# Performance work log

Hardware: AMD Instinct MI355X
Metric: run time of the kernel (lower is better)

## Reference

```python
import jax, jax.numpy as jnp
import numpy as np
from jax import lax

EPS = 1e-10

def _safe_norm(x):
    # torch remove_zeros: replace exact-zero norms with 1e-10
    n = jnp.linalg.norm(x, axis=-1, keepdims=True)
    return jnp.where(n != 0, n, jnp.full_like(n, EPS))

def setup_inputs() -> dict:
    key = jax.random.key(0)
    ks = jax.random.split(key, 5)
    S, B, D = 2048, 32, 512  # seq, batch, 2*hidden
    K = 147  # odd(max_entries/14)
    return {
        "encoder_outputs": jax.random.normal(ks[0], (S, B, D), dtype=jnp.float32),
        "state": jax.random.normal(ks[1], (B, D), dtype=jnp.float32),
        "previous_attention": jax.random.uniform(ks[2], (B, S), dtype=jnp.float32),
        "W_att": jax.random.normal(ks[3], (D, D), dtype=jnp.float32) / np.sqrt(D),
        "b_att": jax.random.normal(ks[4], (D,), dtype=jnp.float32) * 0.01,
        "conv_w": jnp.ones((1, 1, K), dtype=jnp.float32),
        "conv_b": jnp.zeros((1,), dtype=jnp.float32),
    }

def reference(encoder_outputs, state, previous_attention, W_att, b_att, conv_w, conv_b):
    S, B, D = encoder_outputs.shape
    # attended state via linear layer, then cosine-similarity weights (vectorized over seq)
    attended = state @ W_att.T + b_att                       # [B, D]
    ns = attended / _safe_norm(attended)                     # [B, D]
    ne = encoder_outputs / _safe_norm(encoder_outputs)       # [S, B, D]
    weights = jnp.einsum('bd,sbd->bs', ns, ne)               # [B, S]
    # conv1d time smoothing of previous attention (same-length, odd kernel)
    k = conv_w.shape[-1]
    pad = k // 2
    y = lax.conv_general_dilated(previous_attention[:, None, :], conv_w,
                                 window_strides=(1,), padding=[(pad, pad)])
    adjusted = jax.nn.relu(y[:, 0, :] + conv_b)              # [B, S]
    prev_probs = adjusted / jnp.sum(adjusted, axis=1, keepdims=True)
    adj = prev_probs * jax.nn.softmax(weights, axis=1)
    norm_w = adj / jnp.sum(adj, axis=1, keepdims=True)       # [B, S]
    applied = jnp.einsum('bs,sbd->bd', norm_w, encoder_outputs)  # [B, D]
    return applied, norm_w
```

## Files before the change

kernel.cpp:

```cpp
#include <hip/hip_runtime.h>
#include <math.h>


__device__ __forceinline__ float wave_sum(float v) {
    for (int off = 32; off; off >>= 1) v += __shfl_xor(v, off);
    return v;
}

__global__ __launch_bounds__(256) void front_kernel(
    const float* __restrict__ state, const float* __restrict__ W,
    const float* __restrict__ bias, const float* __restrict__ prev,
    const float* __restrict__ cw, const float* __restrict__ cb,
    float* __restrict__ attended, float* __restrict__ adj,
    int S, int D, int K) {
    __shared__ __align__(16) float smem[1024];
    int b = blockIdx.y;
    int t = threadIdx.x;

    if (blockIdx.x < 2) {
        if (t < D / 4)
            ((float4*)smem)[t] = ((const float4*)(state + (size_t)b * D))[t];
        __syncthreads();
        int d = blockIdx.x * 256 + t;
        const float4* Wrow = (const float4*)(W + (size_t)d * D);
        const float4* sv = (const float4*)smem;
        float acc = bias[d];
#pragma unroll 8
        for (int k = 0; k < 128; ++k) {
            float4 w4 = Wrow[k];
            float4 s4 = sv[k];
            acc += w4.x * s4.x + w4.y * s4.y + w4.z * s4.z + w4.w * s4.w;
        }
        attended[(size_t)b * D + d] = acc;
    } else {
        int s0 = (blockIdx.x - 2) * 256;
        int pad = K / 2;
        int seglen = 256 + K - 1;
        float* seg = smem;
        float* wk = smem + 512;
        for (int i = t; i < seglen; i += 256) {
            int s = s0 - pad + i;
            seg[i] = (s >= 0 && s < S) ? prev[(size_t)b * S + s] : 0.f;
        }
        for (int j = t; j < K; j += 256) wk[j] = cw[j];
        __syncthreads();
        float y = cb[0];
        for (int j = 0; j < K; ++j) y += seg[t + j] * wk[j];
        adj[(size_t)b * S + s0 + t] = fmaxf(y, 0.f);
    }
}

__global__ __launch_bounds__(256) void main_kernel(
    const float* __restrict__ e, const float* __restrict__ attended,
    const float* __restrict__ adj, float* __restrict__ partial,
    float* __restrict__ zbuf, float* __restrict__ u,
    int S, int B, int D, int CH) {
    __shared__ __align__(16) float reds[4 * 512 + 4];
    int wave = threadIdx.x >> 6;
    int lane = threadIdx.x & 63;
    int c = blockIdx.x * 4 + wave;
    int b = blockIdx.y;

    const float4* att4 = (const float4*)(attended + (size_t)b * D);
    float4 a0 = att4[lane];
    float4 a1 = att4[lane + 64];
    float asq = a0.x * a0.x + a0.y * a0.y + a0.z * a0.z + a0.w * a0.w
              + a1.x * a1.x + a1.y * a1.y + a1.z * a1.z + a1.w * a1.w;
    asq = wave_sum(asq);
    float an = sqrtf(asq);
    if (an == 0.f) an = 1e-10f;
    float ainv = 1.f / an;
    float4 ns0, ns1;
    ns0.x = a0.x * ainv; ns0.y = a0.y * ainv; ns0.z = a0.z * ainv; ns0.w = a0.w * ainv;
    ns1.x = a1.x * ainv; ns1.y = a1.y * ainv; ns1.z = a1.z * ainv; ns1.w = a1.w * ainv;

    int s0 = c * CH;

    float adjv = 0.f;
    if (CH <= 64 && lane < CH) adjv = adj[(size_t)b * S + s0 + lane];

    float4 acc0 = {0.f, 0.f, 0.f, 0.f};
    float4 acc1 = {0.f, 0.f, 0.f, 0.f};
    float z = 0.f;

    const float4* row4 = (const float4*)(e + ((size_t)s0 * B + b) * D);
    size_t rstride = (size_t)B * D / 4;

    float4 x0 = row4[lane];
    float4 x1 = row4[lane + 64];
    for (int i = 0; i < CH; ++i) {
        float4 nx0, nx1;
        if (i + 1 < CH) {
            nx0 = row4[rstride + lane];
            nx1 = row4[rstride + lane + 64];
        }
        float dot = x0.x * ns0.x + x0.y * ns0.y + x0.z * ns0.z + x0.w * ns0.w
                  + x1.x * ns1.x + x1.y * ns1.y + x1.z * ns1.z + x1.w * ns1.w;
        float sq  = x0.x * x0.x + x0.y * x0.y + x0.z * x0.z + x0.w * x0.w
                  + x1.x * x1.x + x1.y * x1.y + x1.z * x1.z + x1.w * x1.w;
        dot = wave_sum(dot);
        sq  = wave_sum(sq);
        float n = sqrtf(sq);
        if (n == 0.f) n = 1e-10f;
        float w = dot / n;
        float av = (CH <= 64) ? __shfl(adjv, i) : adj[(size_t)b * S + s0 + i];
        float coef = av * __expf(w);
        if (lane == 0) u[(size_t)b * S + s0 + i] = coef;
        acc0.x += coef * x0.x; acc0.y += coef * x0.y;
        acc0.z += coef * x0.z; acc0.w += coef * x0.w;
        acc1.x += coef * x1.x; acc1.y += coef * x1.y;
        acc1.z += coef * x1.z; acc1.w += coef * x1.w;
        z += coef;
        x0 = nx0; x1 = nx1;
        row4 += rstride;
    }

    float* wsl = reds + (wave << 9);
    ((float4*)wsl)[lane] = acc0;
    ((float4*)wsl)[lane + 64] = acc1;
    if (lane == 0) reds[2048 + wave] = z;
    __syncthreads();
    int t = threadIdx.x;
    if (t < 128) {
        const float4* r4 = (const float4*)reds;
        float4 v0 = r4[t];
        float4 v1 = r4[t + 128];
        float4 v2 = r4[t + 256];
        float4 v3 = r4[t + 384];
        float4 o;
        o.x = v0.x + v1.x + v2.x + v3.x;
        o.y = v0.y + v1.y + v2.y + v3.y;
        o.z = v0.z + v1.z + v2.z + v3.z;
        o.w = v0.w + v1.w + v2.w + v3.w;
        ((float4*)(partial + ((size_t)blockIdx.x * B + b) * D))[t] = o;
    }
    if (t == 0)
        zbuf[(size_t)blockIdx.x * B + b] =
            reds[2048] + reds[2049] + reds[2050] + reds[2051];
}

__global__ __launch_bounds__(256) void combine_kernel(
    const float* __restrict__ partial, const float* __restrict__ zbuf,
    const float* __restrict__ u, float* __restrict__ applied,
    float* __restrict__ norm_w, int S, int B, int D, int NPART) {
    int q = blockIdx.x;
    int b = blockIdx.y;
    int t = threadIdx.x;
    __shared__ __align__(16) float4 red4[8][32];
    __shared__ float zsh;

    float zt = (t < NPART) ? zbuf[(size_t)t * B + b] : 0.f;
    zt = wave_sum(zt);
    if (t == 0) zsh = 1.f / zt;

    int c2 = t >> 5;
    int di = t & 31;
    int d4 = q * 32 + di;
    const float4* p4 = (const float4*)partial;
    float4 a = {0.f, 0.f, 0.f, 0.f};
#pragma unroll
    for (int k = 0; k < 4; ++k) {
        float4 x = p4[((size_t)(c2 + (k << 3)) * B + b) * (D >> 2) + d4];
        a.x += x.x; a.y += x.y; a.z += x.z; a.w += x.w;
    }
    red4[c2][di] = a;
    __syncthreads();
    float inv = zsh;
    if (t < 32) {
        float4 s = red4[0][t];
#pragma unroll
        for (int j = 1; j < 8; ++j) {
            float4 x = red4[j][t];
            s.x += x.x; s.y += x.y; s.z += x.z; s.w += x.w;
        }
        s.x *= inv; s.y *= inv; s.z *= inv; s.w *= inv;
        ((float4*)(applied + (size_t)b * D))[q * 32 + t] = s;
    }

    const float4* u4 = (const float4*)(u + (size_t)b * S);
    float4* nw4 = (float4*)(norm_w + (size_t)b * S);
    if (t < 128) {
        int idx = q * (S >> 4) + t;
        float4 x = u4[idx];
        x.x *= inv; x.y *= inv; x.z *= inv; x.w *= inv;
        nw4[idx] = x;
    }
}

extern "C" void kernel_launch(void* const* d_in, const int* in_sizes, int n_in,
                              void* d_out, int out_size, void* d_ws, size_t ws_size,
                              hipStream_t stream) {
    const float* enc   = (const float*)d_in[0];
    const float* state = (const float*)d_in[1];
    const float* prev  = (const float*)d_in[2];
    const float* W     = (const float*)d_in[3];
    const float* bias  = (const float*)d_in[4];
    const float* cw    = (const float*)d_in[5];
    const float* cb    = (const float*)d_in[6];

    const int S = in_sizes[0] / in_sizes[1];
    const int B = in_sizes[2] / S;
    const int D = in_sizes[1] / B;
    const int K = in_sizes[5];

    float* out     = (float*)d_out;
    float* applied = out;
    float* norm_w  = out + (size_t)B * D;

    const int NCHUNK = 128;
    const int CH = S / NCHUNK;
    const int NPART = NCHUNK / 4;

    float* ws       = (float*)d_ws;
    float* attended = ws;
    float* adj      = attended + (size_t)B * D;
    float* u        = adj + (size_t)B * S;
    float* zbuf     = u + (size_t)B * S;
    float* partial  = zbuf + (size_t)NPART * B;

    front_kernel<<<dim3(2 + S / 256, B), 256, 0, stream>>>(
        state, W, bias, prev, cw, cb, attended, adj, S, D, K);
    main_kernel<<<dim3(NPART, B), 256, 0, stream>>>(
        enc, attended, adj, partial, zbuf, u, S, B, D, CH);
    combine_kernel<<<dim3(4, B), 256, 0, stream>>>(
        partial, zbuf, u, applied, norm_w, S, B, D, NPART);
}
```

Baseline: 220.0 us.

## Fuse combine into main kernel via last-block atomic counter, unroll rows by two

Removes the separate combine kernel: each main_kernel block bumps a per-batch atomic counter, and the last block to finish reduces all partials, normalizes, and writes applied and norm_w. The main loop now handles two sequence rows per iteration, interleaving four wave reductions and prefetching two rows ahead. The norm-and-divide is replaced by a hardware rsq. This saves a kernel launch and adds ILP, but the final reduction now runs serially in one block per batch and relies on the counter being reset by front_kernel.

```diff
diff --git a/kernel.cpp b/kernel.cpp
--- a/kernel.cpp
+++ b/kernel.cpp
@@ -12,12 +12,13 @@
     const float* __restrict__ bias, const float* __restrict__ prev,
     const float* __restrict__ cw, const float* __restrict__ cb,
     float* __restrict__ attended, float* __restrict__ adj,
-    int S, int D, int K) {
+    unsigned* __restrict__ counter, int S, int D, int K) {
     __shared__ __align__(16) float smem[1024];
     int b = blockIdx.y;
     int t = threadIdx.x;
 
     if (blockIdx.x < 2) {
+        if (blockIdx.x == 0 && t == 0) counter[b] = 0u;
         if (t < D / 4)
             ((float4*)smem)[t] = ((const float4*)(state + (size_t)b * D))[t];
         __syncthreads();
@@ -54,12 +55,16 @@
     const float* __restrict__ e, const float* __restrict__ attended,
     const float* __restrict__ adj, float* __restrict__ partial,
     float* __restrict__ zbuf, float* __restrict__ u,
-    int S, int B, int D, int CH) {
+    unsigned* __restrict__ counter, float* __restrict__ applied,
+    float* __restrict__ norm_w, int S, int B, int D, int CH) {
     __shared__ __align__(16) float reds[4 * 512 + 4];
+    __shared__ float zsh;
+    __shared__ int is_last;
     int wave = threadIdx.x >> 6;
     int lane = threadIdx.x & 63;
     int c = blockIdx.x * 4 + wave;
     int b = blockIdx.y;
+    int NPART = gridDim.x;
 
     const float4* att4 = (const float4*)(attended + (size_t)b * D);
     float4 a0 = att4[lane];
@@ -76,8 +81,7 @@
 
     int s0 = c * CH;
 
-    float adjv = 0.f;
-    if (CH <= 64 && lane < CH) adjv = adj[(size_t)b * S + s0 + lane];
+    float adjv = (lane < CH) ? adj[(size_t)b * S + s0 + lane] : 0.f;
 
     float4 acc0 = {0.f, 0.f, 0.f, 0.f};
     float4 acc1 = {0.f, 0.f, 0.f, 0.f};
@@ -86,33 +90,52 @@
     const float4* row4 = (const float4*)(e + ((size_t)s0 * B + b) * D);
     size_t rstride = (size_t)B * D / 4;
 
-    float4 x0 = row4[lane];
-    float4 x1 = row4[lane + 64];
-    for (int i = 0; i < CH; ++i) {
-        float4 nx0, nx1;
-        if (i + 1 < CH) {
-            nx0 = row4[rstride + lane];
-            nx1 = row4[rstride + lane + 64];
-        }
-        float dot = x0.x * ns0.x + x0.y * ns0.y + x0.z * ns0.z + x0.w * ns0.w
-                  + x1.x * ns1.x + x1.y * ns1.y + x1.z * ns1.z + x1.w * ns1.w;
-        float sq  = x0.x * x0.x + x0.y * x0.y + x0.z * x0.z + x0.w * x0.w
-                  + x1.x * x1.x + x1.y * x1.y + x1.z * x1.z + x1.w * x1.w;
-        dot = wave_sum(dot);
-        sq  = wave_sum(sq);
-        float n = sqrtf(sq);
-        if (n == 0.f) n = 1e-10f;
-        float w = dot / n;
-        float av = (CH <= 64) ? __shfl(adjv, i) : adj[(size_t)b * S + s0 + i];
-        float coef = av * __expf(w);
-        if (lane == 0) u[(size_t)b * S + s0 + i] = coef;
-        acc0.x += coef * x0.x; acc0.y += coef * x0.y;
-        acc0.z += coef * x0.z; acc0.w += coef * x0.w;
-        acc1.x += coef * x1.x; acc1.y += coef * x1.y;
-        acc1.z += coef * x1.z; acc1.w += coef * x1.w;
-        z += coef;
-        x0 = nx0; x1 = nx1;
-        row4 += rstride;
+    float4 xa0 = row4[lane];
+    float4 xa1 = row4[lane + 64];
+    float4 xb0 = row4[rstride + lane];
+    float4 xb1 = row4[rstride + lane + 64];
+    const float4* pref = row4 + 2 * rstride;
+
+    for (int i = 0; i < CH; i += 2) {
+        float4 pa0, pa1, pb0, pb1;
+        if (i + 2 < CH) {
+            pa0 = pref[lane];           pa1 = pref[lane + 64];
+            pb0 = pref[rstride + lane]; pb1 = pref[rstride + lane + 64];
+        }
+        float ava = __shfl(adjv, i);
+        float avb = __shfl(adjv, i + 1);
+        float dota = xa0.x * ns0.x + xa0.y * ns0.y + xa0.z * ns0.z + xa0.w * ns0.w
+                   + xa1.x * ns1.x + xa1.y * ns1.y + xa1.z * ns1.z + xa1.w * ns1.w;
+        float sqa  = xa0.x * xa0.x + xa0.y * xa0.y + xa0.z * xa0.z + xa0.w * xa0.w
+                   + xa1.x * xa1.x + xa1.y * xa1.y + xa1.z * xa1.z + xa1.w * xa1.w;
+        float dotb = xb0.x * ns0.x + xb0.y * ns0.y + xb0.z * ns0.z + xb0.w * ns0.w
+                   + xb1.x * ns1.x + xb1.y * ns1.y + xb1.z * ns1.z + xb1.w * ns1.w;
+        float sqb  = xb0.x * xb0.x + xb0.y * xb0.y + xb0.z * xb0.z + xb0.w * xb0.w
+                   + xb1.x * xb1.x + xb1.y * xb1.y + xb1.z * xb1.z + xb1.w * xb1.w;
+#pragma unroll
+        for (int off = 32; off; off >>= 1) {
+            dota += __shfl_xor(dota, off);
+            dotb += __shfl_xor(dotb, off);
+            sqa  += __shfl_xor(sqa, off);
+            sqb  += __shfl_xor(sqb, off);
+        }
+        float ra = (sqa > 0.f) ? __builtin_amdgcn_rsqf(sqa) : 0.f;
+        float rb = (sqb > 0.f) ? __builtin_amdgcn_rsqf(sqb) : 0.f;
+        float coefa = ava * __expf(dota * ra);
+        float coefb = avb * __expf(dotb * rb);
+        if (lane == 0)
+            *((float2*)(u + (size_t)b * S + s0 + i)) = make_float2(coefa, coefb);
+        acc0.x += coefa * xa0.x + coefb * xb0.x;
+        acc0.y += coefa * xa0.y + coefb * xb0.y;
+        acc0.z += coefa * xa0.z + coefb * xb0.z;
+        acc0.w += coefa * xa0.w + coefb * xb0.w;
+        acc1.x += coefa * xa1.x + coefb * xb1.x;
+        acc1.y += coefa * xa1.y + coefb * xb1.y;
+        acc1.z += coefa * xa1.z + coefb * xb1.z;
+        acc1.w += coefa * xa1.w + coefb * xb1.w;
+        z += coefa + coefb;
+        xa0 = pa0; xa1 = pa1; xb0 = pb0; xb1 = pb1;
+        pref += 2 * rstride;
     }
 
     float* wsl = reds + (wave << 9);
@@ -137,50 +160,37 @@
     if (t == 0)
         zbuf[(size_t)blockIdx.x * B + b] =
             reds[2048] + reds[2049] + reds[2050] + reds[2051];
-}
-
-__global__ __launch_bounds__(256) void combine_kernel(
-    const float* __restrict__ partial, const float* __restrict__ zbuf,
-    const float* __restrict__ u, float* __restrict__ applied,
-    float* __restrict__ norm_w, int S, int B, int D, int NPART) {
-    int q = blockIdx.x;
-    int b = blockIdx.y;
-    int t = threadIdx.x;
-    __shared__ __align__(16) float4 red4[8][32];
-    __shared__ float zsh;
+
+    __syncthreads();
+    if (t == 0) {
+        __threadfence();
+        unsigned old = atomicAdd(counter + b, 1u);
+        is_last = (old == (unsigned)(NPART - 1)) ? 1 : 0;
+    }
+    __syncthreads();
+    if (!is_last) return;
+    __threadfence();
 
     float zt = (t < NPART) ? zbuf[(size_t)t * B + b] : 0.f;
     zt = wave_sum(zt);
     if (t == 0) zsh = 1.f / zt;
-
-    int c2 = t >> 5;
-    int di = t & 31;
-    int d4 = q * 32 + di;
-    const float4* p4 = (const float4*)partial;
-    float4 a = {0.f, 0.f, 0.f, 0.f};
-#pragma unroll
-    for (int k = 0; k < 4; ++k) {
-        float4 x = p4[((size_t)(c2 + (k << 3)) * B + b) * (D >> 2) + d4];
-        a.x += x.x; a.y += x.y; a.z += x.z; a.w += x.w;
-    }
-    red4[c2][di] = a;
     __syncthreads();
     float inv = zsh;
-    if (t < 32) {
-        float4 s = red4[0][t];
-#pragma unroll
-        for (int j = 1; j < 8; ++j) {
-            float4 x = red4[j][t];
-            s.x += x.x; s.y += x.y; s.z += x.z; s.w += x.w;
-        }
-        s.x *= inv; s.y *= inv; s.z *= inv; s.w *= inv;
-        ((float4*)(applied + (size_t)b * D))[q * 32 + t] = s;
+
+    if (t < 128) {
+        float4 a = {0.f, 0.f, 0.f, 0.f};
+        const float4* p4 = (const float4*)partial;
+        for (int cix = 0; cix < NPART; ++cix) {
+            float4 x = p4[((size_t)cix * B + b) * (D >> 2) + t];
+            a.x += x.x; a.y += x.y; a.z += x.z; a.w += x.w;
+        }
+        a.x *= inv; a.y *= inv; a.z *= inv; a.w *= inv;
+        ((float4*)(applied + (size_t)b * D))[t] = a;
     }
 
     const float4* u4 = (const float4*)(u + (size_t)b * S);
     float4* nw4 = (float4*)(norm_w + (size_t)b * S);
-    if (t < 128) {
-        int idx = q * (S >> 4) + t;
+    for (int idx = t; idx < (S >> 2); idx += 256) {
         float4 x = u4[idx];
         x.x *= inv; x.y *= inv; x.z *= inv; x.w *= inv;
         nw4[idx] = x;
@@ -217,11 +227,11 @@
     float* u        = adj + (size_t)B * S;
     float* zbuf     = u + (size_t)B * S;
     float* partial  = zbuf + (size_t)NPART * B;
+    unsigned* counter = (unsigned*)(partial + (size_t)NPART * B * D);
 
     front_kernel<<<dim3(2 + S / 256, B), 256, 0, stream>>>(
-        state, W, bias, prev, cw, cb, attended, adj, S, D, K);
+        state, W, bias, prev, cw, cb, attended, adj, counter, S, D, K);
     main_kernel<<<dim3(NPART, B), 256, 0, stream>>>(
-        enc, attended, adj, partial, zbuf, u, S, B, D, CH);
-    combine_kernel<<<dim3(4, B), 256, 0, stream>>>(
-        partial, zbuf, u, applied, norm_w, S, B, D, NPART);
-}
+        enc, attended, adj, partial, zbuf, u, counter, applied, norm_w,
+        S, B, D, CH);
+}
```

New measurement: 275.5 us. +25.2%, slower.
